# Optimization experiments

Measured on AMD Instinct MI355X. Metric: run time of the kernel, lower is better.

## Reference

```python
import jax, jax.numpy as jnp
import numpy as np

DIM = 384
HEADS = 12
WH, WW = 7, 7
N = WH * WW  # 49
B_ = 4096


def _relative_position_index():
    coords = np.stack(np.meshgrid(np.arange(WH), np.arange(WW), indexing='ij'))  # [2,WH,WW]
    flat = coords.reshape(2, -1)                       # [2, N]
    rel = flat[:, :, None] - flat[:, None, :]          # [2, N, N]
    rel = rel.transpose(1, 2, 0)                       # [N, N, 2]
    rel[:, :, 0] += WH - 1
    rel[:, :, 1] += WW - 1
    rel[:, :, 0] *= 2 * WW - 1
    return jnp.asarray(rel.sum(-1), dtype=jnp.int32)   # [N, N]


def setup_inputs() -> dict:
    key = jax.random.key(0)
    ks = jax.random.split(key, 6)
    x = jax.random.normal(ks[0], (B_, N, DIM), dtype=jnp.float32)
    qkv_w = jax.random.normal(ks[1], (3 * DIM, DIM), dtype=jnp.float32) * 0.02
    qkv_b = jnp.zeros((3 * DIM,), dtype=jnp.float32)
    proj_w = jax.random.normal(ks[2], (DIM, DIM), dtype=jnp.float32) * 0.02
    proj_b = jnp.zeros((DIM,), dtype=jnp.float32)
    rpb_table = jax.random.normal(ks[3], ((2 * WH - 1) * (2 * WW - 1), HEADS), dtype=jnp.float32) * 0.02
    rel_index = _relative_position_index()
    return {"x": x, "qkv_w": qkv_w, "qkv_b": qkv_b, "proj_w": proj_w,
            "proj_b": proj_b, "rpb_table": rpb_table, "rel_index": rel_index}


def reference(x, qkv_w, qkv_b, proj_w, proj_b, rpb_table, rel_index):
    B, n, C = x.shape
    hd = C // HEADS
    scale = hd ** (-0.5)
    qkv = x @ qkv_w.T + qkv_b                      # [B, N, 3C]
    qkv = qkv.reshape(B, n, 3, HEADS, hd)
    q = qkv[:, :, 0].transpose(0, 2, 1, 3) * scale  # [B, H, N, hd]
    k = qkv[:, :, 1].transpose(0, 2, 1, 3)
    v = qkv[:, :, 2].transpose(0, 2, 1, 3)
    attn = jnp.einsum('bhnd,bhmd->bhnm', q, k)      # [B, H, N, N]
    bias = rpb_table[rel_index]                     # [N, N, H]
    attn = attn + bias.transpose(2, 0, 1)[None]     # broadcast over B
    attn = jax.nn.softmax(attn, axis=-1)
    out = jnp.einsum('bhnm,bhmd->bhnd', attn, v)    # [B, H, N, hd]
    out = out.transpose(0, 2, 1, 3).reshape(B, n, C)
    return out @ proj_w.T + proj_b
```

## Files before the change

kernel.cpp:

```cpp
#include <hip/hip_runtime.h>

typedef __attribute__((ext_vector_type(8))) short bf16x8;
typedef __attribute__((ext_vector_type(4))) float f32x4;
typedef unsigned short u16;
typedef unsigned int u32;

#define NW 49
#define NP 64
#define CDIM 384
#define NHEAD 12
#define HDIM 32
#define XS_STRIDE 392
#define QK_STRIDE 40
#define VT_STRIDE 72
#define P_STRIDE 72
#define LDS_BYTES 159744

__device__ __forceinline__ u16 f2bf(float f) {
  u32 u = __float_as_uint(f);
  u32 r = u + 0x7fffu + ((u >> 16) & 1u);
  return (u16)(r >> 16);
}

__global__ void prep_kernel(const float* __restrict__ qkv_w,
                            const float* __restrict__ proj_w,
                            const float* __restrict__ rpb,
                            const int* __restrict__ rel,
                            u16* __restrict__ wq, u16* __restrict__ wp,
                            float* __restrict__ bias) {
  int i = blockIdx.x * 256 + threadIdx.x;
  if (i < 1152 * 384) wq[i] = f2bf(qkv_w[i]);
  if (i < 384 * 384) wp[i] = f2bf(proj_w[i]);
  if (i < 12 * 2401) {
    int h = i / 2401, nm = i % 2401;
    bias[i] = rpb[rel[nm] * 12 + h];
  }
}

__global__ __launch_bounds__(256, 1)
void wattn_kernel(const float* __restrict__ x,
                  const float* __restrict__ qkv_b,
                  const float* __restrict__ proj_b,
                  const u16* __restrict__ wq,
                  const u16* __restrict__ wp,
                  const float* __restrict__ bias,
                  float* __restrict__ out) {
  extern __shared__ u16 lds[];
  const int b = blockIdx.x;
  const int tid = threadIdx.x;
  const int wid = tid >> 6;
  const int lane = tid & 63;
  const int lr = lane & 15;
  const int lg = lane >> 4;

  u16* xs = lds;
  u16* ao = lds + NP * XS_STRIDE;
  u16* wb = lds + 2 * NP * XS_STRIDE + wid * 7424;
  u16* Qb = wb;
  u16* Kb = wb + NP * QK_STRIDE;
  u16* Vt = wb + 2 * NP * QK_STRIDE;
  u16* Pb = Qb;

  const float* xb = x + (size_t)b * (NW * CDIM);
  for (int i = tid; i < 15 * XS_STRIDE; i += 256) xs[49 * XS_STRIDE + i] = 0;
  for (int i = tid; i < 49 * 96; i += 256) {
    int r = i / 96, c4 = i % 96;
    float4 v = ((const float4*)xb)[i];
    ushort4 uu;
    uu.x = f2bf(v.x); uu.y = f2bf(v.y); uu.z = f2bf(v.z); uu.w = f2bf(v.w);
    *(ushort4*)&xs[r * XS_STRIDE + c4 * 4] = uu;
  }
  __syncthreads();

  const f32x4 fzero = {0.f, 0.f, 0.f, 0.f};
  const float scale = 0.17677669529663687f;

  for (int g = 0; g < 3; ++g) {
    const int h = g * 4 + wid;

    int jrow[6];
#pragma unroll
    for (int nt = 0; nt < 6; ++nt)
      jrow[nt] = (nt >> 1) * CDIM + h * HDIM + (nt & 1) * 16 + lr;

    f32x4 acc[4][6];
#pragma unroll
    for (int mt = 0; mt < 4; ++mt)
#pragma unroll
      for (int nt = 0; nt < 6; ++nt) acc[mt][nt] = fzero;

    bf16x8 aA[4], bA[6], aB[4], bB[6];
    {
      int k0 = lg * 8;
#pragma unroll
      for (int mt = 0; mt < 4; ++mt) aA[mt] = *(const bf16x8*)&xs[(mt * 16 + lr) * XS_STRIDE + k0];
#pragma unroll
      for (int nt = 0; nt < 6; ++nt) bA[nt] = *(const bf16x8*)&wq[jrow[nt] * CDIM + k0];
    }
#pragma unroll
    for (int kk = 0; kk < 6; ++kk) {
      {
        int k0 = (2 * kk + 1) * 32 + lg * 8;
#pragma unroll
        for (int mt = 0; mt < 4; ++mt) aB[mt] = *(const bf16x8*)&xs[(mt * 16 + lr) * XS_STRIDE + k0];
#pragma unroll
        for (int nt = 0; nt < 6; ++nt) bB[nt] = *(const bf16x8*)&wq[jrow[nt] * CDIM + k0];
      }
#pragma unroll
      for (int nt = 0; nt < 6; ++nt)
#pragma unroll
        for (int mt = 0; mt < 4; ++mt)
          acc[mt][nt] = __builtin_amdgcn_mfma_f32_16x16x32_bf16(aA[mt], bA[nt], acc[mt][nt], 0, 0, 0);
      if (kk < 5) {
        int k0 = (2 * kk + 2) * 32 + lg * 8;
#pragma unroll
        for (int mt = 0; mt < 4; ++mt) aA[mt] = *(const bf16x8*)&xs[(mt * 16 + lr) * XS_STRIDE + k0];
#pragma unroll
        for (int nt = 0; nt < 6; ++nt) bA[nt] = *(const bf16x8*)&wq[jrow[nt] * CDIM + k0];
      }
#pragma unroll
      for (int nt = 0; nt < 6; ++nt)
#pragma unroll
        for (int mt = 0; mt < 4; ++mt)
          acc[mt][nt] = __builtin_amdgcn_mfma_f32_16x16x32_bf16(aB[mt], bB[nt], acc[mt][nt], 0, 0, 0);
    }

#pragma unroll
    for (int nt = 0; nt < 6; ++nt) {
      float qb = qkv_b[jrow[nt]];
#pragma unroll
      for (int mt = 0; mt < 4; ++mt) {
#pragma unroll
        for (int r = 0; r < 4; ++r) {
          float v = acc[mt][nt][r] + qb;
          int tok = mt * 16 + lg * 4 + r;
          int d = (nt & 1) * 16 + lr;
          if (nt < 2)      Qb[tok * QK_STRIDE + d] = f2bf(v * scale);
          else if (nt < 4) Kb[tok * QK_STRIDE + d] = f2bf(v);
          else             Vt[d * VT_STRIDE + tok] = f2bf(v);
        }
      }
    }

    bf16x8 qf[4], kf[4];
#pragma unroll
    for (int t = 0; t < 4; ++t) {
      qf[t] = *(const bf16x8*)&Qb[(t * 16 + lr) * QK_STRIDE + lg * 8];
      kf[t] = *(const bf16x8*)&Kb[(t * 16 + lr) * QK_STRIDE + lg * 8];
    }
    f32x4 S[4][4];
#pragma unroll
    for (int mt = 0; mt < 4; ++mt)
#pragma unroll
      for (int nt = 0; nt < 4; ++nt)
        S[mt][nt] = __builtin_amdgcn_mfma_f32_16x16x32_bf16(qf[mt], kf[nt], fzero, 0, 0, 0);

    const float* bh = bias + h * 2401;
#pragma unroll
    for (int mt = 0; mt < 4; ++mt) {
#pragma unroll
      for (int nt = 0; nt < 4; ++nt) {
        int m = nt * 16 + lr;
#pragma unroll
        for (int r = 0; r < 4; ++r) {
          int n = mt * 16 + lg * 4 + r;
          float s = S[mt][nt][r];
          S[mt][nt][r] = (m < NW && n < NW) ? s + bh[n * NW + m] : -1e30f;
        }
      }
#pragma unroll
      for (int r = 0; r < 4; ++r) {
        float mx = fmaxf(fmaxf(S[mt][0][r], S[mt][1][r]), fmaxf(S[mt][2][r], S[mt][3][r]));
        mx = fmaxf(mx, __shfl_xor(mx, 1));
        mx = fmaxf(mx, __shfl_xor(mx, 2));
        mx = fmaxf(mx, __shfl_xor(mx, 4));
        mx = fmaxf(mx, __shfl_xor(mx, 8));
        float sum = 0.f;
#pragma unroll
        for (int nt = 0; nt < 4; ++nt) {
          float e = __expf(S[mt][nt][r] - mx);
          S[mt][nt][r] = e; sum += e;
        }
        sum += __shfl_xor(sum, 1);
        sum += __shfl_xor(sum, 2);
        sum += __shfl_xor(sum, 4);
        sum += __shfl_xor(sum, 8);
        float inv = 1.0f / sum;
#pragma unroll
        for (int nt = 0; nt < 4; ++nt) S[mt][nt][r] *= inv;
      }
#pragma unroll
      for (int nt = 0; nt < 4; ++nt)
#pragma unroll
        for (int r = 0; r < 4; ++r)
          Pb[(lg * 4 + r) * P_STRIDE + nt * 16 + lr] = f2bf(S[mt][nt][r]);
      bf16x8 pf0 = *(const bf16x8*)&Pb[lr * P_STRIDE + lg * 8];
      bf16x8 pf1 = *(const bf16x8*)&Pb[lr * P_STRIDE + 32 + lg * 8];
#pragma unroll
      for (int vt = 0; vt < 2; ++vt) {
        bf16x8 v0 = *(const bf16x8*)&Vt[(vt * 16 + lr) * VT_STRIDE + lg * 8];
        bf16x8 v1 = *(const bf16x8*)&Vt[(vt * 16 + lr) * VT_STRIDE + 32 + lg * 8];
        f32x4 o = __builtin_amdgcn_mfma_f32_16x16x32_bf16(pf0, v0, fzero, 0, 0, 0);
        o = __builtin_amdgcn_mfma_f32_16x16x32_bf16(pf1, v1, o, 0, 0, 0);
#pragma unroll
        for (int r = 0; r < 4; ++r)
          ao[(mt * 16 + lg * 4 + r) * XS_STRIDE + h * HDIM + vt * 16 + lr] = f2bf(o[r]);
      }
    }
  }
  __syncthreads();

  f32x4 oacc[4][6];
#pragma unroll
  for (int mt = 0; mt < 4; ++mt)
#pragma unroll
    for (int n6 = 0; n6 < 6; ++n6) oacc[mt][n6] = fzero;

  const int jbase = wid * 96;
  bf16x8 aA2[4], bA2[6], aB2[4], bB2[6];
  {
    int k0 = lg * 8;
#pragma unroll
    for (int mt = 0; mt < 4; ++mt) aA2[mt] = *(const bf16x8*)&ao[(mt * 16 + lr) * XS_STRIDE + k0];
#pragma unroll
    for (int n6 = 0; n6 < 6; ++n6) bA2[n6] = *(const bf16x8*)&wp[(jbase + n6 * 16 + lr) * CDIM + k0];
  }
#pragma unroll
  for (int kk = 0; kk < 6; ++kk) {
    {
      int k0 = (2 * kk + 1) * 32 + lg * 8;
#pragma unroll
      for (int mt = 0; mt < 4; ++mt) aB2[mt] = *(const bf16x8*)&ao[(mt * 16 + lr) * XS_STRIDE + k0];
#pragma unroll
      for (int n6 = 0; n6 < 6; ++n6) bB2[n6] = *(const bf16x8*)&wp[(jbase + n6 * 16 + lr) * CDIM + k0];
    }
#pragma unroll
    for (int n6 = 0; n6 < 6; ++n6)
#pragma unroll
      for (int mt = 0; mt < 4; ++mt)
        oacc[mt][n6] = __builtin_amdgcn_mfma_f32_16x16x32_bf16(aA2[mt], bA2[n6], oacc[mt][n6], 0, 0, 0);
    if (kk < 5) {
      int k0 = (2 * kk + 2) * 32 + lg * 8;
#pragma unroll
      for (int mt = 0; mt < 4; ++mt) aA2[mt] = *(const bf16x8*)&ao[(mt * 16 + lr) * XS_STRIDE + k0];
#pragma unroll
      for (int n6 = 0; n6 < 6; ++n6) bA2[n6] = *(const bf16x8*)&wp[(jbase + n6 * 16 + lr) * CDIM + k0];
    }
#pragma unroll
    for (int n6 = 0; n6 < 6; ++n6)
#pragma unroll
      for (int mt = 0; mt < 4; ++mt)
        oacc[mt][n6] = __builtin_amdgcn_mfma_f32_16x16x32_bf16(aB2[mt], bB2[n6], oacc[mt][n6], 0, 0, 0);
  }

  float* ob = out + (size_t)b * (NW * CDIM);
#pragma unroll
  for (int n6 = 0; n6 < 6; ++n6) {
    int j = jbase + n6 * 16 + lr;
    float pbv = proj_b[j];
#pragma unroll
    for (int mt = 0; mt < 4; ++mt)
#pragma unroll
      for (int r = 0; r < 4; ++r) {
        int tok = mt * 16 + lg * 4 + r;
        if (tok < NW) ob[(size_t)tok * CDIM + j] = oacc[mt][n6][r] + pbv;
      }
  }
}

extern "C" void kernel_launch(void* const* d_in, const int* in_sizes, int n_in,
                              void* d_out, int out_size, void* d_ws, size_t ws_size,
                              hipStream_t stream) {
  const float* x      = (const float*)d_in[0];
  const float* qkv_w  = (const float*)d_in[1];
  const float* qkv_b  = (const float*)d_in[2];
  const float* proj_w = (const float*)d_in[3];
  const float* proj_b = (const float*)d_in[4];
  const float* rpb    = (const float*)d_in[5];
  const int*   rel    = (const int*)d_in[6];
  float* out = (float*)d_out;

  u16* wq = (u16*)d_ws;
  u16* wp = (u16*)((char*)d_ws + 884736);
  float* bias = (float*)((char*)d_ws + 1179648);

  int nB = in_sizes[0] / (NW * CDIM);

  prep_kernel<<<dim3((1152 * 384 + 255) / 256), dim3(256), 0, stream>>>(
      qkv_w, proj_w, rpb, rel, wq, wp, bias);

  (void)hipFuncSetAttribute((const void*)wattn_kernel,
                            hipFuncAttributeMaxDynamicSharedMemorySize, LDS_BYTES);
  wattn_kernel<<<dim3(nB), dim3(256), LDS_BYTES, stream>>>(
      x, qkv_b, proj_b, wq, wp, bias, out);
}
```

Baseline: 1.589 ms.

## Split output projection into separate kernel to cut LDS and raise occupancy

The fused window-attention kernel is split in two. The attention kernel now writes fp32 per-head outputs to global memory instead of an LDS tile. A new projection kernel does the output GEMM over flat 64-row tiles and writes its result in place into the same buffer. Per-wave scratch is shrunk by aliasing the Q, K, V and P buffers, so LDS drops enough for two blocks per CU (launch bounds 2). MFMA sections are wrapped in s_setprio hints. The cost is an extra global round trip of the attention output in fp32 plus a second kernel launch, and proj_kernel assumes the total row count (4096×49) divides evenly by 64.

```diff
diff --git a/kernel.cpp b/kernel.cpp
--- a/kernel.cpp
+++ b/kernel.cpp
@@ -14,7 +14,8 @@
 #define QK_STRIDE 40
 #define VT_STRIDE 72
 #define P_STRIDE 72
-#define LDS_BYTES 159744
+#define WB_U16 3456
+#define LDS_A_BYTES (NP * XS_STRIDE * 2 + 4 * WB_U16 * 2)
 
 __device__ __forceinline__ u16 f2bf(float f) {
   u32 u = __float_as_uint(f);
@@ -37,14 +38,12 @@
   }
 }
 
-__global__ __launch_bounds__(256, 1)
-void wattn_kernel(const float* __restrict__ x,
-                  const float* __restrict__ qkv_b,
-                  const float* __restrict__ proj_b,
-                  const u16* __restrict__ wq,
-                  const u16* __restrict__ wp,
-                  const float* __restrict__ bias,
-                  float* __restrict__ out) {
+__global__ __launch_bounds__(256, 2)
+void wattn2_kernel(const float* __restrict__ x,
+                   const float* __restrict__ qkv_b,
+                   const u16* __restrict__ wq,
+                   const float* __restrict__ bias,
+                   float* __restrict__ aout) {
   extern __shared__ u16 lds[];
   const int b = blockIdx.x;
   const int tid = threadIdx.x;
@@ -54,12 +53,10 @@
   const int lg = lane >> 4;
 
   u16* xs = lds;
-  u16* ao = lds + NP * XS_STRIDE;
-  u16* wb = lds + 2 * NP * XS_STRIDE + wid * 7424;
-  u16* Qb = wb;
-  u16* Kb = wb + NP * QK_STRIDE;
-  u16* Vt = wb + 2 * NP * QK_STRIDE;
-  u16* Pb = Qb;
+  u16* wb = lds + NP * XS_STRIDE + wid * WB_U16;
+  u16* QK = wb;
+  u16* Vt = wb;
+  u16* Pb = wb + 2304;
 
   const float* xb = x + (size_t)b * (NW * CDIM);
   for (int i = tid; i < 15 * XS_STRIDE; i += 256) xs[49 * XS_STRIDE + i] = 0;
@@ -106,11 +103,13 @@
 #pragma unroll
         for (int nt = 0; nt < 6; ++nt) bB[nt] = *(const bf16x8*)&wq[jrow[nt] * CDIM + k0];
       }
+      __builtin_amdgcn_s_setprio(1);
 #pragma unroll
       for (int nt = 0; nt < 6; ++nt)
 #pragma unroll
         for (int mt = 0; mt < 4; ++mt)
           acc[mt][nt] = __builtin_amdgcn_mfma_f32_16x16x32_bf16(aA[mt], bA[nt], acc[mt][nt], 0, 0, 0);
+      __builtin_amdgcn_s_setprio(0);
       if (kk < 5) {
         int k0 = (2 * kk + 2) * 32 + lg * 8;
 #pragma unroll
@@ -118,44 +117,68 @@
 #pragma unroll
         for (int nt = 0; nt < 6; ++nt) bA[nt] = *(const bf16x8*)&wq[jrow[nt] * CDIM + k0];
       }
+      __builtin_amdgcn_s_setprio(1);
 #pragma unroll
       for (int nt = 0; nt < 6; ++nt)
 #pragma unroll
         for (int mt = 0; mt < 4; ++mt)
           acc[mt][nt] = __builtin_amdgcn_mfma_f32_16x16x32_bf16(aB[mt], bB[nt], acc[mt][nt], 0, 0, 0);
-    }
-
-#pragma unroll
-    for (int nt = 0; nt < 6; ++nt) {
+      __builtin_amdgcn_s_setprio(0);
+    }
+
+#pragma unroll
+    for (int nt = 0; nt < 2; ++nt) {
       float qb = qkv_b[jrow[nt]];
 #pragma unroll
-      for (int mt = 0; mt < 4; ++mt) {
-#pragma unroll
-        for (int r = 0; r < 4; ++r) {
-          float v = acc[mt][nt][r] + qb;
+      for (int mt = 0; mt < 4; ++mt)
+#pragma unroll
+        for (int r = 0; r < 4; ++r) {
+          int tok = mt * 16 + lg * 4 + r;
+          QK[tok * QK_STRIDE + (nt & 1) * 16 + lr] = f2bf((acc[mt][nt][r] + qb) * scale);
+        }
+    }
+    bf16x8 qf[4], kf[4];
+#pragma unroll
+    for (int t = 0; t < 4; ++t)
+      qf[t] = *(const bf16x8*)&QK[(t * 16 + lr) * QK_STRIDE + lg * 8];
+#pragma unroll
+    for (int nt = 2; nt < 4; ++nt) {
+      float qb = qkv_b[jrow[nt]];
+#pragma unroll
+      for (int mt = 0; mt < 4; ++mt)
+#pragma unroll
+        for (int r = 0; r < 4; ++r) {
+          int tok = mt * 16 + lg * 4 + r;
+          QK[tok * QK_STRIDE + (nt & 1) * 16 + lr] = f2bf(acc[mt][nt][r] + qb);
+        }
+    }
+#pragma unroll
+    for (int t = 0; t < 4; ++t)
+      kf[t] = *(const bf16x8*)&QK[(t * 16 + lr) * QK_STRIDE + lg * 8];
+#pragma unroll
+    for (int nt = 4; nt < 6; ++nt) {
+      float qb = qkv_b[jrow[nt]];
+#pragma unroll
+      for (int mt = 0; mt < 4; ++mt)
+#pragma unroll
+        for (int r = 0; r < 4; ++r) {
           int tok = mt * 16 + lg * 4 + r;
           int d = (nt & 1) * 16 + lr;
-          if (nt < 2)      Qb[tok * QK_STRIDE + d] = f2bf(v * scale);
-          else if (nt < 4) Kb[tok * QK_STRIDE + d] = f2bf(v);
-          else             Vt[d * VT_STRIDE + tok] = f2bf(v);
-        }
-      }
-    }
-
-    bf16x8 qf[4], kf[4];
-#pragma unroll
-    for (int t = 0; t < 4; ++t) {
-      qf[t] = *(const bf16x8*)&Qb[(t * 16 + lr) * QK_STRIDE + lg * 8];
-      kf[t] = *(const bf16x8*)&Kb[(t * 16 + lr) * QK_STRIDE + lg * 8];
-    }
+          Vt[d * VT_STRIDE + tok] = f2bf(acc[mt][nt][r] + qb);
+        }
+    }
+
     f32x4 S[4][4];
+    __builtin_amdgcn_s_setprio(1);
 #pragma unroll
     for (int mt = 0; mt < 4; ++mt)
 #pragma unroll
       for (int nt = 0; nt < 4; ++nt)
         S[mt][nt] = __builtin_amdgcn_mfma_f32_16x16x32_bf16(qf[mt], kf[nt], fzero, 0, 0, 0);
+    __builtin_amdgcn_s_setprio(0);
 
     const float* bh = bias + h * 2401;
+    float* ob = aout + (size_t)b * (NW * CDIM) + h * HDIM;
 #pragma unroll
     for (int mt = 0; mt < 4; ++mt) {
 #pragma unroll
@@ -200,16 +223,43 @@
       for (int vt = 0; vt < 2; ++vt) {
         bf16x8 v0 = *(const bf16x8*)&Vt[(vt * 16 + lr) * VT_STRIDE + lg * 8];
         bf16x8 v1 = *(const bf16x8*)&Vt[(vt * 16 + lr) * VT_STRIDE + 32 + lg * 8];
+        __builtin_amdgcn_s_setprio(1);
         f32x4 o = __builtin_amdgcn_mfma_f32_16x16x32_bf16(pf0, v0, fzero, 0, 0, 0);
         o = __builtin_amdgcn_mfma_f32_16x16x32_bf16(pf1, v1, o, 0, 0, 0);
-#pragma unroll
-        for (int r = 0; r < 4; ++r)
-          ao[(mt * 16 + lg * 4 + r) * XS_STRIDE + h * HDIM + vt * 16 + lr] = f2bf(o[r]);
-      }
-    }
+        __builtin_amdgcn_s_setprio(0);
+#pragma unroll
+        for (int r = 0; r < 4; ++r) {
+          int tok = mt * 16 + lg * 4 + r;
+          if (tok < NW) ob[(size_t)tok * CDIM + vt * 16 + lr] = o[r];
+        }
+      }
+    }
+  }
+}
+
+__global__ __launch_bounds__(256, 2)
+void proj_kernel(const u16* __restrict__ wp,
+                 const float* __restrict__ proj_b,
+                 float* __restrict__ io) {
+  __shared__ u16 As[NP * XS_STRIDE];
+  const int tid = threadIdx.x;
+  const int wid = tid >> 6;
+  const int lane = tid & 63;
+  const int lr = lane & 15;
+  const int lg = lane >> 4;
+  const int m0 = blockIdx.x * 64;
+
+  const float* src = io + (size_t)m0 * CDIM;
+  for (int i = tid; i < 64 * 96; i += 256) {
+    int r = i / 96, c4 = i % 96;
+    float4 v = ((const float4*)src)[i];
+    ushort4 uu;
+    uu.x = f2bf(v.x); uu.y = f2bf(v.y); uu.z = f2bf(v.z); uu.w = f2bf(v.w);
+    *(ushort4*)&As[r * XS_STRIDE + c4 * 4] = uu;
   }
   __syncthreads();
 
+  const f32x4 fzero = {0.f, 0.f, 0.f, 0.f};
   f32x4 oacc[4][6];
 #pragma unroll
   for (int mt = 0; mt < 4; ++mt)
@@ -221,7 +271,7 @@
   {
     int k0 = lg * 8;
 #pragma unroll
-    for (int mt = 0; mt < 4; ++mt) aA2[mt] = *(const bf16x8*)&ao[(mt * 16 + lr) * XS_STRIDE + k0];
+    for (int mt = 0; mt < 4; ++mt) aA2[mt] = *(const bf16x8*)&As[(mt * 16 + lr) * XS_STRIDE + k0];
 #pragma unroll
     for (int n6 = 0; n6 < 6; ++n6) bA2[n6] = *(const bf16x8*)&wp[(jbase + n6 * 16 + lr) * CDIM + k0];
   }
@@ -230,30 +280,34 @@
     {
       int k0 = (2 * kk + 1) * 32 + lg * 8;
 #pragma unroll
-      for (int mt = 0; mt < 4; ++mt) aB2[mt] = *(const bf16x8*)&ao[(mt * 16 + lr) * XS_STRIDE + k0];
+      for (int mt = 0; mt < 4; ++mt) aB2[mt] = *(const bf16x8*)&As[(mt * 16 + lr) * XS_STRIDE + k0];
 #pragma unroll
       for (int n6 = 0; n6 < 6; ++n6) bB2[n6] = *(const bf16x8*)&wp[(jbase + n6 * 16 + lr) * CDIM + k0];
     }
+    __builtin_amdgcn_s_setprio(1);
 #pragma unroll
     for (int n6 = 0; n6 < 6; ++n6)
 #pragma unroll
       for (int mt = 0; mt < 4; ++mt)
         oacc[mt][n6] = __builtin_amdgcn_mfma_f32_16x16x32_bf16(aA2[mt], bA2[n6], oacc[mt][n6], 0, 0, 0);
+    __builtin_amdgcn_s_setprio(0);
     if (kk < 5) {
       int k0 = (2 * kk + 2) * 32 + lg * 8;
 #pragma unroll
-      for (int mt = 0; mt < 4; ++mt) aA2[mt] = *(const bf16x8*)&ao[(mt * 16 + lr) * XS_STRIDE + k0];
+      for (int mt = 0; mt < 4; ++mt) aA2[mt] = *(const bf16x8*)&As[(mt * 16 + lr) * XS_STRIDE + k0];
 #pragma unroll
       for (int n6 = 0; n6 < 6; ++n6) bA2[n6] = *(const bf16x8*)&wp[(jbase + n6 * 16 + lr) * CDIM + k0];
     }
+    __builtin_amdgcn_s_setprio(1);
 #pragma unroll
     for (int n6 = 0; n6 < 6; ++n6)
 #pragma unroll
       for (int mt = 0; mt < 4; ++mt)
         oacc[mt][n6] = __builtin_amdgcn_mfma_f32_16x16x32_bf16(aB2[mt], bB2[n6], oacc[mt][n6], 0, 0, 0);
-  }
-
-  float* ob = out + (size_t)b * (NW * CDIM);
+    __builtin_amdgcn_s_setprio(0);
+  }
+
+  float* ob = io + (size_t)m0 * CDIM;
 #pragma unroll
   for (int n6 = 0; n6 < 6; ++n6) {
     int j = jbase + n6 * 16 + lr;
@@ -263,7 +317,7 @@
 #pragma unroll
       for (int r = 0; r < 4; ++r) {
         int tok = mt * 16 + lg * 4 + r;
-        if (tok < NW) ob[(size_t)tok * CDIM + j] = oacc[mt][n6][r] + pbv;
+        ob[(size_t)tok * CDIM + j] = oacc[mt][n6][r] + pbv;
       }
   }
 }
@@ -285,12 +339,16 @@
   float* bias = (float*)((char*)d_ws + 1179648);
 
   int nB = in_sizes[0] / (NW * CDIM);
+  int nRows = in_sizes[0] / CDIM;
+  int nB2 = nRows / 64;
 
   prep_kernel<<<dim3((1152 * 384 + 255) / 256), dim3(256), 0, stream>>>(
       qkv_w, proj_w, rpb, rel, wq, wp, bias);
 
-  (void)hipFuncSetAttribute((const void*)wattn_kernel,
-                            hipFuncAttributeMaxDynamicSharedMemorySize, LDS_BYTES);
-  wattn_kernel<<<dim3(nB), dim3(256), LDS_BYTES, stream>>>(
-      x, qkv_b, proj_b, wq, wp, bias, out);
-}
+  (void)hipFuncSetAttribute((const void*)wattn2_kernel,
+                            hipFuncAttributeMaxDynamicSharedMemorySize, LDS_A_BYTES);
+  wattn2_kernel<<<dim3(nB), dim3(256), LDS_A_BYTES, stream>>>(
+      x, qkv_b, wq, bias, out);
+
+  proj_kernel<<<dim3(nB2), dim3(256), 0, stream>>>(wp, proj_b, out);
+}
```

Result: faster. 1.466 ms (-7.7%).
